# Performance work log

Measured on AMD Instinct MI355X. Metric: run time of the kernel, lower is better.

The kernel has to match this reference:

```python
import jax, jax.numpy as jnp
import numpy as np

EPS = 1e-9
LAM_SEL, LAM_ID, LAM_RATE, LAM_KL, LAM_ENT, LAM_SMOOTH = 1.0, 10.0, 5.0, 0.1, 0.05, 0.5


def setup_inputs() -> dict:
    T, BS, V, K, RIDS = 48, 256, 4096, 32, 1024
    key = jax.random.key(0)
    ks = jax.random.split(key, 10)
    selector_logits = jax.random.normal(ks[0], (BS, 2, K), dtype=jnp.float32)
    selector_probs = jax.nn.softmax(jax.random.normal(ks[1], (BS, 2, K)), axis=-1)
    sel_idx = jax.random.randint(ks[2], (BS, 2), 0, K)
    selector_onehot = jax.nn.one_hot(sel_idx, K, dtype=jnp.float32)
    out_ids = jax.nn.softmax(jax.random.normal(ks[3], (T, BS, V)), axis=-1)
    out_rates = jax.random.uniform(ks[4], (T, BS, 1), dtype=jnp.float32)
    lab_idx = jax.random.randint(ks[5], (T + 2, BS), 0, V)
    trg_labels = jax.nn.one_hot(lab_idx, V, dtype=jnp.float32)
    trg_rates = jax.random.uniform(ks[6], (T + 2, BS, 1), dtype=jnp.float32)
    trg_lengths = jax.random.randint(ks[7], (BS,), 4, T + 2).astype(jnp.int32)
    candi_ids = jax.random.randint(ks[8], (BS, 2, K), 0, RIDS).astype(jnp.int32)
    routes = jax.random.randint(ks[9], (BS, V), 0, RIDS).astype(jnp.int32)
    return {
        'selector_logits': selector_logits, 'selector_probs': selector_probs,
        'selector_onehot': selector_onehot, 'out_ids': out_ids, 'out_rates': out_rates,
        'trg_labels': trg_labels, 'trg_rates': trg_rates, 'trg_lengths': trg_lengths,
        'candi_ids': candi_ids, 'routes': routes,
    }


def _align(lab, T_pred):
    T_lab = lab.shape[0]
    if T_lab >= T_pred + 2:
        return lab[1:-1]
    elif T_lab == T_pred:
        return lab
    else:
        pad = T_pred - T_lab
        return jnp.concatenate([lab, jnp.repeat(lab[-1:], pad, axis=0)], axis=0)


def _loss(selector_logits, selector_probs, selector_onehot, out_ids, out_rates,
          trg_labels, trg_rates, trg_lengths, candi_ids, routes):
    bs, _, K = selector_probs.shape
    # --- selector NLL (use_bce_logits=False path) ---
    sel_mask = (selector_onehot.sum(-1) > 0.5).astype(jnp.float32)      # [bs,2]
    sel_p_true = jnp.maximum((selector_probs * selector_onehot).sum(-1), EPS)
    loss_sel = (-jnp.log(sel_p_true) * sel_mask).sum() / jnp.maximum(sel_mask.sum(), 1.0)

    # --- id NLL over aligned target labels ---
    T_pred = out_ids.shape[0]
    tla = _align(trg_labels, T_pred)                                    # [T,bs,V]
    tra = _align(trg_rates, T_pred)                                     # [T,bs,1]
    step_mask = (tla.sum(-1) > 0.5).astype(jnp.float32)                 # [T,bs]
    p_true = jnp.maximum((out_ids * tla).sum(-1), EPS)
    loss_id = (-jnp.log(p_true) * step_mask).sum() * LAM_ID / jnp.maximum(step_mask.sum(), 1.0)

    # --- rate L1 ---
    denom_rate = jnp.maximum(1, (trg_lengths - 2).sum()).astype(jnp.float32)
    loss_rate = jnp.abs(out_rates - tra).sum() * LAM_RATE / denom_rate

    # --- KL over per-batch candidate unions (vectorized dedup via first-occurrence) ---
    U2 = 2 * K
    ids = candi_ids.reshape(bs, U2)                                     # [bs,2K]
    probs_flat = selector_probs.reshape(bs, U2)                         # [bs,2K]
    eq = ids[:, :, None] == ids[:, None, :]                             # [bs,2K,2K]
    rep = jnp.argmax(eq, axis=-1)                                       # first occurrence idx
    slots = jnp.arange(U2)
    valid = (rep == slots[None, :]).astype(jnp.float32)                 # [bs,2K] union slots
    Ucnt = valid.sum(-1)                                                # [bs]
    # Pm: scatter-add selector probs onto union slots (duplicates summed)
    rep_oh = (rep[:, :, None] == slots[None, None, :]).astype(jnp.float32)  # [bs,2K,2K]
    Pm = jnp.einsum('biu,bi->bu', rep_oh, probs_flat)                   # [bs,2K]
    Pm = Pm / jnp.maximum(Pm.sum(-1, keepdims=True), EPS)
    # Pb: project route mass onto union ids
    dist_r = out_ids.sum(0)                                             # [bs,V]
    match = (routes[:, :, None] == ids[:, None, :]).astype(jnp.float32)  # [bs,V,2K]
    agg = jnp.einsum('bvu,bv->bu', match, dist_r) * valid               # [bs,2K]
    s = agg.sum(-1, keepdims=True)                                      # [bs,1]
    uniform = valid / jnp.maximum(Ucnt, 1.0)[:, None]
    Pb = jnp.where(s > 0, agg / jnp.maximum(s, EPS), uniform)
    Pb_c = jnp.maximum(Pb, EPS)
    kl_b = (Pb_c * (jnp.log(Pb_c) - jnp.log(jnp.maximum(Pm, EPS))) * valid).sum(-1)
    loss_kl = LAM_KL * (kl_b.sum() / max(1, bs))

    # --- entropy of selector probs ---
    p = jnp.maximum(selector_probs, EPS)                                # [bs,2,K]
    ent_b = 0.5 * (-(p * jnp.log(p)).sum(-1)).sum(-1)                   # [bs]
    loss_entropy = LAM_ENT * (ent_b.sum() / max(1, bs))

    # --- rate smoothness ---
    r = out_rates[..., 0]                                               # [T,bs]
    dr = jnp.abs(r[1:] - r[:-1])                                        # [T-1,bs]
    eff = jnp.maximum(trg_lengths - 3, 0)                               # [bs]
    smask = (jnp.arange(T_pred - 1)[:, None] < eff[None, :]).astype(jnp.float32)
    loss_smooth = LAM_SMOOTH * (dr * smask).sum()

    return LAM_SEL * loss_sel + loss_id + loss_rate + loss_kl + loss_entropy + loss_smooth


def reference(selector_logits, selector_probs, selector_onehot, out_ids, out_rates,
              trg_labels, trg_rates, trg_lengths, candi_ids, routes):
    return _loss(selector_logits, selector_probs, selector_onehot, out_ids, out_rates,
                 trg_labels, trg_rates, trg_lengths, candi_ids, routes)
```

## Files before the change

### kernel.cpp

```cpp
#include <hip/hip_runtime.h>
#include <math.h>

#define EPSF 1e-9f

typedef float v4f __attribute__((ext_vector_type(4)));


__global__ __launch_bounds__(256) void e2e3_prep(
    const float* __restrict__ selector_probs,
    const int*   __restrict__ candi_ids,
    const int*   __restrict__ routes,
    float* __restrict__ pmlog_g,
    float* __restrict__ valid_g,
    signed char* __restrict__ slot_map,
    float* __restrict__ agg_g,
    float* __restrict__ acc)
{
    const int b   = blockIdx.x;
    const int tid = threadIdx.x;

    __shared__ int   ids_s[64];
    __shared__ int   table[1024];
    __shared__ int   rep_s[64];

    if (tid < 64) agg_g[b * 64 + tid] = 0.f;
    if (b == 0 && tid < 4) acc[tid] = 0.f;

    for (int i = tid; i < 1024; i += 256) table[i] = 64;
    if (tid < 64) ids_s[tid] = candi_ids[b * 64 + tid];
    __syncthreads();
    if (tid < 64) atomicMin(&table[ids_s[tid]], tid);
    __syncthreads();
    if (tid < 64) {
        const int r = table[ids_s[tid]];
        rep_s[tid] = r;
        valid_g[b * 64 + tid] = (r == tid) ? 1.f : 0.f;
    }
    __syncthreads();
    if (tid < 64) {
        float pm = 0.f;
        for (int i = 0; i < 64; ++i)
            if (rep_s[i] == tid) pm += selector_probs[b * 64 + i];
        float tot = pm;
        #pragma unroll
        for (int off = 32; off >= 1; off >>= 1) tot += __shfl_xor(tot, off, 64);
        pm = pm / fmaxf(tot, EPSF);
        pmlog_g[b * 64 + tid] = logf(fmaxf(pm, EPSF));
    }

    const int4* rp = reinterpret_cast<const int4*>(routes + (size_t)b * 4096 + tid * 16);
    signed char smv[16];
    #pragma unroll
    for (int j = 0; j < 4; ++j) {
        const int4 rv = rp[j];
        const int t0 = table[rv.x], t1 = table[rv.y], t2 = table[rv.z], t3 = table[rv.w];
        smv[j * 4 + 0] = (signed char)(t0 < 64 ? t0 : -1);
        smv[j * 4 + 1] = (signed char)(t1 < 64 ? t1 : -1);
        smv[j * 4 + 2] = (signed char)(t2 < 64 ? t2 : -1);
        smv[j * 4 + 3] = (signed char)(t3 < 64 ? t3 : -1);
    }
    *reinterpret_cast<int4*>(slot_map + (size_t)b * 4096 + tid * 16) =
        *reinterpret_cast<const int4*>(smv);
}

__global__ __launch_bounds__(512) void e2e3_stream(
    const float* __restrict__ out_ids,
    const float* __restrict__ trg_labels,
    const signed char* __restrict__ slot_map,
    float* __restrict__ agg_g,
    float* __restrict__ acc)
{
    const int bid  = blockIdx.x;
    const int tid  = threadIdx.x;
    const int wave = tid >> 6;
    const int lane = tid & 63;

    const int b = (bid >> 1) & 255;
    const int v = (bid & 1) * 2048 + tid * 4;

    __shared__ float agg_s[64];
    __shared__ float red[2][8];
    if (tid < 64) agg_s[tid] = 0.f;
    __syncthreads();

    const unsigned int sm =
        *reinterpret_cast<const unsigned int*>(slot_map + (size_t)b * 4096 + v);
    const int u0 = (int)(signed char)(sm & 0xFF);
    const int u1 = (int)(signed char)((sm >> 8) & 0xFF);
    const int u2 = (int)(signed char)((sm >> 16) & 0xFF);
    const int u3 = (int)(signed char)((sm >> 24) & 0xFF);

    const size_t STEP = (size_t)2097152;
    const size_t e0   = (size_t)(bid * 512 + tid) * 4;
    const float* op = out_ids + e0;
    const float* lp = trg_labels + e0 + 1048576;

    float s0 = 0.f, s1 = 0.f, s2 = 0.f, s3 = 0.f;
    float idnum = 0.f, idcnt = 0.f;

    v4f oa = *reinterpret_cast<const v4f*>(op);
    v4f la = __builtin_nontemporal_load(reinterpret_cast<const v4f*>(lp));
    v4f ob = *reinterpret_cast<const v4f*>(op + STEP);
    v4f lb = __builtin_nontemporal_load(reinterpret_cast<const v4f*>(lp + STEP));

    for (int s = 0; s < 24; ++s) {
        v4f oc = (v4f)(0.f), lc = (v4f)(0.f);
        if (s < 22) {
            oc = *reinterpret_cast<const v4f*>(op + (size_t)(s + 2) * STEP);
            lc = __builtin_nontemporal_load(
                     reinterpret_cast<const v4f*>(lp + (size_t)(s + 2) * STEP));
        }
        s0 += oa.x; s1 += oa.y; s2 += oa.z; s3 += oa.w;
        if (la.x > 0.5f) { idnum -= logf(fmaxf(oa.x, EPSF)); idcnt += 1.f; }
        if (la.y > 0.5f) { idnum -= logf(fmaxf(oa.y, EPSF)); idcnt += 1.f; }
        if (la.z > 0.5f) { idnum -= logf(fmaxf(oa.z, EPSF)); idcnt += 1.f; }
        if (la.w > 0.5f) { idnum -= logf(fmaxf(oa.w, EPSF)); idcnt += 1.f; }
        oa = ob; la = lb; ob = oc; lb = lc;
    }

    if (u0 >= 0) atomicAdd(&agg_s[u0], s0);
    if (u1 >= 0) atomicAdd(&agg_s[u1], s1);
    if (u2 >= 0) atomicAdd(&agg_s[u2], s2);
    if (u3 >= 0) atomicAdd(&agg_s[u3], s3);

    #pragma unroll
    for (int off = 32; off >= 1; off >>= 1) {
        idnum += __shfl_down(idnum, off, 64);
        idcnt += __shfl_down(idcnt, off, 64);
    }
    if (lane == 0) { red[0][wave] = idnum; red[1][wave] = idcnt; }
    __syncthreads();
    if (tid == 0) {
        float a = 0.f, c = 0.f;
        #pragma unroll
        for (int w = 0; w < 8; ++w) { a += red[0][w]; c += red[1][w]; }
        atomicAdd(&acc[0], a);
        atomicAdd(&acc[1], c);
    }
    if (tid < 64) atomicAdd(&agg_g[b * 64 + tid], agg_s[tid]);
}

__global__ __launch_bounds__(64) void e2e3_kl2(
    const float* __restrict__ agg_g,
    const float* __restrict__ pmlog_g,
    const float* __restrict__ valid_g,
    float* __restrict__ acc)
{
    const int b = blockIdx.x;
    const int u = threadIdx.x;

    const float va = valid_g[b * 64 + u];
    const float a  = (va > 0.5f) ? agg_g[b * 64 + u] : 0.f;
    float s = a, uc = va;
    #pragma unroll
    for (int off = 32; off >= 1; off >>= 1) {
        s  += __shfl_xor(s,  off, 64);
        uc += __shfl_xor(uc, off, 64);
    }
    const float pb = (s > 0.f) ? (a / fmaxf(s, EPSF)) : (va / fmaxf(uc, 1.f));
    float term = 0.f;
    if (va > 0.5f) {
        const float pbc = fmaxf(pb, EPSF);
        term = pbc * (logf(pbc) - pmlog_g[b * 64 + u]);
    }
    #pragma unroll
    for (int off = 32; off >= 1; off >>= 1) term += __shfl_down(term, off, 64);
    if (u == 0) atomicAdd(&acc[2], term);
}

__global__ __launch_bounds__(256) void e2e3_small(
    const float* __restrict__ selector_probs,
    const float* __restrict__ selector_onehot,
    const float* __restrict__ out_rates,
    const float* __restrict__ trg_rates,
    const int*   __restrict__ trg_lengths,
    const float* __restrict__ acc,
    float* __restrict__ out)
{
    const int tid  = threadIdx.x;
    const int wave = tid >> 6;
    const int lane = tid & 63;

    float v_selnum = 0.f, v_selcnt = 0.f, v_ent = 0.f;
    float v_rate = 0.f, v_den = 0.f, v_smooth = 0.f;

    for (int g = tid; g < 512; g += 256) {
        const float* pp = selector_probs  + g * 32;
        const float* oo = selector_onehot + g * 32;
        float p = 0.f, m = 0.f;
        #pragma unroll
        for (int k = 0; k < 32; ++k) { p += pp[k] * oo[k]; m += oo[k]; }
        if (m > 0.5f) { v_selnum += -logf(fmaxf(p, EPSF)); v_selcnt += 1.f; }
    }
    for (int i = tid; i < 256 * 64; i += 256) {
        const float p = fmaxf(selector_probs[i], EPSF);
        v_ent += -p * logf(p);
    }
    for (int i = tid; i < 48 * 256; i += 256)
        v_rate += fabsf(out_rates[i] - trg_rates[i + 256]);
    for (int b2 = tid; b2 < 256; b2 += 256)
        v_den += (float)(trg_lengths[b2] - 2);
    for (int i = tid; i < 47 * 256; i += 256) {
        const int b2 = i & 255;
        const int t  = i >> 8;
        int eff = trg_lengths[b2] - 3; if (eff < 0) eff = 0;
        if (t < eff) v_smooth += fabsf(out_rates[i + 256] - out_rates[i]);
    }

    __shared__ float red[6][4];
    float vals[6] = {v_selnum, v_selcnt, v_ent, v_rate, v_den, v_smooth};
    #pragma unroll
    for (int k = 0; k < 6; ++k) {
        float v = vals[k];
        #pragma unroll
        for (int off = 32; off >= 1; off >>= 1) v += __shfl_down(v, off, 64);
        if (lane == 0) red[k][wave] = v;
    }
    __syncthreads();
    if (tid == 0) {
        float s[6];
        #pragma unroll
        for (int k = 0; k < 6; ++k) s[k] = red[k][0] + red[k][1] + red[k][2] + red[k][3];
        const float loss =
              s[0] / fmaxf(s[1], 1.f)
            + 10.f * acc[0] / fmaxf(acc[1], 1.f)
            + 5.f  * s[3]   / fmaxf(s[4], 1.f)
            + 0.1f * acc[2] * (1.f / 256.f)
            + 0.05f * 0.5f * s[2] * (1.f / 256.f)
            + 0.5f * s[5];
        out[0] = loss;
    }
}

extern "C" void kernel_launch(void* const* d_in, const int* in_sizes, int n_in,
                              void* d_out, int out_size, void* d_ws, size_t ws_size,
                              hipStream_t stream) {
    const float* selector_probs  = (const float*)d_in[1];
    const float* selector_onehot = (const float*)d_in[2];
    const float* out_ids         = (const float*)d_in[3];
    const float* out_rates       = (const float*)d_in[4];
    const float* trg_labels      = (const float*)d_in[5];
    const float* trg_rates       = (const float*)d_in[6];
    const int*   trg_lengths     = (const int*)d_in[7];
    const int*   candi_ids       = (const int*)d_in[8];
    const int*   routes          = (const int*)d_in[9];

    char* ws = (char*)d_ws;
    float*       acc      = (float*)ws;
    float*       agg_g    = (float*)(ws + 256);
    float*       pmlog_g  = (float*)(ws + 256 + 65536);
    float*       valid_g  = (float*)(ws + 256 + 131072);
    signed char* slot_map = (signed char*)(ws + 196864);

    e2e3_prep<<<256, 256, 0, stream>>>(selector_probs, candi_ids, routes,
                                       pmlog_g, valid_g, slot_map,
                                       agg_g, acc);
    e2e3_stream<<<1024, 512, 0, stream>>>(out_ids, trg_labels, slot_map,
                                          agg_g, acc);
    e2e3_kl2<<<256, 64, 0, stream>>>(agg_g, pmlog_g, valid_g, acc);
    e2e3_small<<<1, 256, 0, stream>>>(selector_probs, selector_onehot,
                                      out_rates, trg_rates, trg_lengths,
                                      acc, (float*)d_out);
}
```

Baseline: 116.3 us.

## Remove prep kernel by building dedup table inside stream and KL kernels

Drops the separate prep kernel. Each stream block now builds the candidate-id dedup table in shared memory and maps its routes directly, and the KL kernel recomputes validity and the merged-probability log itself. Workspace zeroing moves to a hipMemsetAsync. This removes one kernel launch and the slot_map, pmlog and valid round trips through global memory. In exchange every stream block repeats the table build (an extra sync plus an atomicMin pass), and a memset operation is added to the stream.

```diff
diff --git a/kernel.cpp b/kernel.cpp
--- a/kernel.cpp
+++ b/kernel.cpp
@@ -5,68 +5,12 @@
 
 typedef float v4f __attribute__((ext_vector_type(4)));
 
-
-__global__ __launch_bounds__(256) void e2e3_prep(
-    const float* __restrict__ selector_probs,
-    const int*   __restrict__ candi_ids,
-    const int*   __restrict__ routes,
-    float* __restrict__ pmlog_g,
-    float* __restrict__ valid_g,
-    signed char* __restrict__ slot_map,
-    float* __restrict__ agg_g,
-    float* __restrict__ acc)
-{
-    const int b   = blockIdx.x;
-    const int tid = threadIdx.x;
-
-    __shared__ int   ids_s[64];
-    __shared__ int   table[1024];
-    __shared__ int   rep_s[64];
-
-    if (tid < 64) agg_g[b * 64 + tid] = 0.f;
-    if (b == 0 && tid < 4) acc[tid] = 0.f;
-
-    for (int i = tid; i < 1024; i += 256) table[i] = 64;
-    if (tid < 64) ids_s[tid] = candi_ids[b * 64 + tid];
-    __syncthreads();
-    if (tid < 64) atomicMin(&table[ids_s[tid]], tid);
-    __syncthreads();
-    if (tid < 64) {
-        const int r = table[ids_s[tid]];
-        rep_s[tid] = r;
-        valid_g[b * 64 + tid] = (r == tid) ? 1.f : 0.f;
-    }
-    __syncthreads();
-    if (tid < 64) {
-        float pm = 0.f;
-        for (int i = 0; i < 64; ++i)
-            if (rep_s[i] == tid) pm += selector_probs[b * 64 + i];
-        float tot = pm;
-        #pragma unroll
-        for (int off = 32; off >= 1; off >>= 1) tot += __shfl_xor(tot, off, 64);
-        pm = pm / fmaxf(tot, EPSF);
-        pmlog_g[b * 64 + tid] = logf(fmaxf(pm, EPSF));
-    }
-
-    const int4* rp = reinterpret_cast<const int4*>(routes + (size_t)b * 4096 + tid * 16);
-    signed char smv[16];
-    #pragma unroll
-    for (int j = 0; j < 4; ++j) {
-        const int4 rv = rp[j];
-        const int t0 = table[rv.x], t1 = table[rv.y], t2 = table[rv.z], t3 = table[rv.w];
-        smv[j * 4 + 0] = (signed char)(t0 < 64 ? t0 : -1);
-        smv[j * 4 + 1] = (signed char)(t1 < 64 ? t1 : -1);
-        smv[j * 4 + 2] = (signed char)(t2 < 64 ? t2 : -1);
-        smv[j * 4 + 3] = (signed char)(t3 < 64 ? t3 : -1);
-    }
-    *reinterpret_cast<int4*>(slot_map + (size_t)b * 4096 + tid * 16) =
-        *reinterpret_cast<const int4*>(smv);
-}
 
 __global__ __launch_bounds__(512) void e2e3_stream(
     const float* __restrict__ out_ids,
     const float* __restrict__ trg_labels,
-    const signed char* __restrict__ slot_map,
+    const int*   __restrict__ candi_ids,
+    const int*   __restrict__ routes,
     float* __restrict__ agg_g,
     float* __restrict__ acc)
 {
@@ -78,17 +22,20 @@
     const int b = (bid >> 1) & 255;
     const int v = (bid & 1) * 2048 + tid * 4;
 
+    __shared__ int   table[1024];
     __shared__ float agg_s[64];
     __shared__ float red[2][8];
+
+    table[tid]       = 64;
+    table[tid + 512] = 64;
     if (tid < 64) agg_s[tid] = 0.f;
     __syncthreads();
-
-    const unsigned int sm =
-        *reinterpret_cast<const unsigned int*>(slot_map + (size_t)b * 4096 + v);
-    const int u0 = (int)(signed char)(sm & 0xFF);
-    const int u1 = (int)(signed char)((sm >> 8) & 0xFF);
-    const int u2 = (int)(signed char)((sm >> 16) & 0xFF);
-    const int u3 = (int)(signed char)((sm >> 24) & 0xFF);
+    if (tid < 64) atomicMin(&table[candi_ids[b * 64 + tid]], tid);
+    __syncthreads();
+
+    const int4 rt = *reinterpret_cast<const int4*>(routes + (size_t)b * 4096 + v);
+    const int tu0 = table[rt.x], tu1 = table[rt.y];
+    const int tu2 = table[rt.z], tu3 = table[rt.w];
 
     const size_t STEP = (size_t)2097152;
     const size_t e0   = (size_t)(bid * 512 + tid) * 4;
@@ -118,10 +65,10 @@
         oa = ob; la = lb; ob = oc; lb = lc;
     }
 
-    if (u0 >= 0) atomicAdd(&agg_s[u0], s0);
-    if (u1 >= 0) atomicAdd(&agg_s[u1], s1);
-    if (u2 >= 0) atomicAdd(&agg_s[u2], s2);
-    if (u3 >= 0) atomicAdd(&agg_s[u3], s3);
+    if (tu0 < 64) atomicAdd(&agg_s[tu0], s0);
+    if (tu1 < 64) atomicAdd(&agg_s[tu1], s1);
+    if (tu2 < 64) atomicAdd(&agg_s[tu2], s2);
+    if (tu3 < 64) atomicAdd(&agg_s[tu3], s3);
 
     #pragma unroll
     for (int off = 32; off >= 1; off >>= 1) {
@@ -141,16 +88,38 @@
 }
 
 __global__ __launch_bounds__(64) void e2e3_kl2(
+    const float* __restrict__ selector_probs,
+    const int*   __restrict__ candi_ids,
     const float* __restrict__ agg_g,
-    const float* __restrict__ pmlog_g,
-    const float* __restrict__ valid_g,
     float* __restrict__ acc)
 {
     const int b = blockIdx.x;
     const int u = threadIdx.x;
 
-    const float va = valid_g[b * 64 + u];
-    const float a  = (va > 0.5f) ? agg_g[b * 64 + u] : 0.f;
+    __shared__ int table[1024];
+    __shared__ int ids_s[64];
+    __shared__ int rep_s[64];
+
+    #pragma unroll
+    for (int i = 0; i < 16; ++i) table[u + i * 64] = 64;
+    ids_s[u] = candi_ids[b * 64 + u];
+    __syncthreads();
+    atomicMin(&table[ids_s[u]], u);
+    __syncthreads();
+    const int rep = table[ids_s[u]];
+    rep_s[u] = rep;
+    const float va = (rep == u) ? 1.f : 0.f;
+    __syncthreads();
+
+    float pm = 0.f;
+    for (int i = 0; i < 64; ++i)
+        if (rep_s[i] == u) pm += selector_probs[b * 64 + i];
+    float tot = pm;
+    #pragma unroll
+    for (int off = 32; off >= 1; off >>= 1) tot += __shfl_xor(tot, off, 64);
+    const float pmlog = logf(fmaxf(pm / fmaxf(tot, EPSF), EPSF));
+
+    const float a = (va > 0.5f) ? agg_g[b * 64 + u] : 0.f;
     float s = a, uc = va;
     #pragma unroll
     for (int off = 32; off >= 1; off >>= 1) {
@@ -161,7 +130,7 @@
     float term = 0.f;
     if (va > 0.5f) {
         const float pbc = fmaxf(pb, EPSF);
-        term = pbc * (logf(pbc) - pmlog_g[b * 64 + u]);
+        term = pbc * (logf(pbc) - pmlog);
     }
     #pragma unroll
     for (int off = 32; off >= 1; off >>= 1) term += __shfl_down(term, off, 64);
@@ -245,19 +214,15 @@
     const int*   candi_ids       = (const int*)d_in[8];
     const int*   routes          = (const int*)d_in[9];
 
-    char* ws = (char*)d_ws;
-    float*       acc      = (float*)ws;
-    float*       agg_g    = (float*)(ws + 256);
-    float*       pmlog_g  = (float*)(ws + 256 + 65536);
-    float*       valid_g  = (float*)(ws + 256 + 131072);
-    signed char* slot_map = (signed char*)(ws + 196864);
-
-    e2e3_prep<<<256, 256, 0, stream>>>(selector_probs, candi_ids, routes,
-                                       pmlog_g, valid_g, slot_map,
-                                       agg_g, acc);
-    e2e3_stream<<<1024, 512, 0, stream>>>(out_ids, trg_labels, slot_map,
-                                          agg_g, acc);
-    e2e3_kl2<<<256, 64, 0, stream>>>(agg_g, pmlog_g, valid_g, acc);
+    char*  ws    = (char*)d_ws;
+    float* acc   = (float*)ws;
+    float* agg_g = (float*)(ws + 256);
+
+    (void)hipMemsetAsync(ws, 0, 256 + 65536, stream);
+
+    e2e3_stream<<<1024, 512, 0, stream>>>(out_ids, trg_labels, candi_ids,
+                                          routes, agg_g, acc);
+    e2e3_kl2<<<256, 64, 0, stream>>>(selector_probs, candi_ids, agg_g, acc);
     e2e3_small<<<1, 256, 0, stream>>>(selector_probs, selector_onehot,
                                       out_rates, trg_rates, trg_lengths,
                                       acc, (float*)d_out);
```

Measured after the change: 119.5 us. 2.8% more time.
